# Optimization experiments

Measured on AMD Instinct MI355X. Metric: run time of the kernel, lower is better.

The kernel has to match this reference:

```python
import jax, jax.numpy as jnp
import numpy as np

B, IN_DIM, H, L, P = 256, 64, 768, 4, 8
EPS = 1e-5


def _layernorm(h, g, b):
    mu = jnp.mean(h, axis=-1, keepdims=True)
    var = jnp.mean((h - mu) ** 2, axis=-1, keepdims=True)
    return (h - mu) * jax.lax.rsqrt(var + EPS) * g + b


def setup_inputs() -> dict:
    key = jax.random.key(0)
    ks = jax.random.split(key, 20)
    s_in = 1.0 / np.sqrt(IN_DIM)
    s_h = 1.0 / np.sqrt(H)
    return {
        "x": jax.random.normal(ks[0], (B, IN_DIM), jnp.float32),
        "w_in": jax.random.normal(ks[1], (IN_DIM, H), jnp.float32) * s_in,
        "b_in": jnp.zeros((H,), jnp.float32),
        "ln_g": jnp.ones((L, H), jnp.float32),
        "ln_b": jnp.zeros((L, H), jnp.float32),
        "trop_w": jax.random.normal(ks[2], (L, H, H), jnp.float32) * s_h,  # [L, out, in]
        "trop_b": jnp.zeros((L, H), jnp.float32),
        "lf_amax": jax.random.normal(ks[3], (L, H, P), jnp.float32) * 0.5 + 1.0,
        "lf_bmax": jax.random.normal(ks[4], (L, H, P), jnp.float32) * 0.1,
        "lf_amin": jax.random.normal(ks[5], (L, H, P), jnp.float32) * 0.5 + 1.0,
        "lf_bmin": jax.random.normal(ks[6], (L, H, P), jnp.float32) * 0.1,
        "lf_alpha": jnp.zeros((L, H), jnp.float32),
        "gate_w": jax.random.normal(ks[7], (L, H, H), jnp.float32) * 0.02,
        "gate_b": jnp.full((L, H), 2.0, jnp.float32),
        "cls_w": jax.random.normal(ks[8], (L, H, H), jnp.float32) * s_h,
        "cls_b": jnp.zeros((L, H), jnp.float32),
        "out_g": jnp.ones((H,), jnp.float32),
        "out_b": jnp.zeros((H,), jnp.float32),
        "head_w": jax.random.normal(ks[9], (H, 1), jnp.float32) * s_h,
        "head_b": jnp.zeros((1,), jnp.float32),
    }


def reference(x, w_in, b_in, ln_g, ln_b, trop_w, trop_b, lf_amax, lf_bmax,
              lf_amin, lf_bmin, lf_alpha, gate_w, gate_b, cls_w, cls_b,
              out_g, out_b, head_w, head_b):
    h = x @ w_in + b_in  # [B, H]
    for l in range(L):
        res = h
        hn = _layernorm(h, ln_g[l], ln_b[l])
        # Tropical (max-plus) linear: y[b,o] = max_i(hn[b,i] + W[o,i]) + bias[o]
        t = jnp.max(hn[:, None, :] + trop_w[l][None, :, :], axis=-1) + trop_b[l]
        # LF dual activation: blend of convex (max-plus) and concave (min-plus) PWL
        fmax = jnp.max(t[..., None] * lf_amax[l] + lf_bmax[l], axis=-1)  # [B, H]
        fmin = jnp.min(t[..., None] * lf_amin[l] + lf_bmin[l], axis=-1)
        a = jax.nn.sigmoid(lf_alpha[l])
        trop_out = a * fmax + (1.0 - a) * fmin
        class_out = jax.nn.gelu(hn @ cls_w[l] + cls_b[l], approximate=False)
        g = jax.nn.sigmoid(hn @ gate_w[l] + gate_b[l])
        h = res + g * trop_out + (1.0 - g) * class_out
    h = _layernorm(h, out_g, out_b)
    return (h @ head_w + head_b).squeeze(-1)  # [B]
```

## Files before the change

### kernel.cpp

```cpp
#include <hip/hip_runtime.h>
#include <math.h>

#define HDIM 768
#define BDIM 256
#define INDIM 64
#define NLAYERS 4
#define PDIM 8
#define KSPLIT 16
#define KLEN 48
#define CHK 16
#define TR 128
#define TC 64
#define NTROPBLK 384
#define NCGBLK 96

typedef short bf16x8 __attribute__((ext_vector_type(8)));
typedef float f32x4 __attribute__((ext_vector_type(4)));

__device__ __forceinline__ float sigmoidf_(float x) { return 1.f / (1.f + expf(-x)); }
__device__ __forceinline__ float geluf_(float x) { return 0.5f * x * (1.f + erff(x * 0.70710678118654752f)); }
__device__ __forceinline__ unsigned short f2bf(float f) {
    unsigned int u = __float_as_uint(f);
    u += 0x7FFFu + ((u >> 16) & 1u);
    return (unsigned short)(u >> 16);
}

__device__ __forceinline__ void gload_lds16(const float* g, float* l) {
    __builtin_amdgcn_global_load_lds((const __attribute__((address_space(1))) void*)g,
                                     (__attribute__((address_space(3))) void*)l, 16, 0, 0);
}

__global__ __launch_bounds__(256) void prep_k(const float* __restrict__ trop_w,
                                              const float* __restrict__ cls_w,
                                              const float* __restrict__ gate_w,
                                              float* __restrict__ twT,
                                              unsigned short* __restrict__ wB)
{
    __shared__ float tile[64][65];
    const int z = blockIdx.z;
    const int a0 = blockIdx.x * 64;
    const int b0 = blockIdx.y * 64;
    const int c = threadIdx.x & 63;
    const int r4 = threadIdx.x >> 6;

    if (z < NLAYERS) {
        const float* s = trop_w + (size_t)z * HDIM * HDIM;
        float* d = twT + (size_t)z * HDIM * HDIM;
#pragma unroll
        for (int it = 0; it < 16; ++it) {
            const int r = it * 4 + r4;
            tile[r][c] = s[(size_t)(a0 + r) * HDIM + b0 + c];
        }
        __syncthreads();
#pragma unroll
        for (int it = 0; it < 16; ++it) {
            const int r = it * 4 + r4;
            d[(size_t)(b0 + r) * HDIM + a0 + c] = tile[c][r];
        }
    } else {
        const int zz = z - NLAYERS;
        const int l = zz >> 1, mat = zz & 1;
        const float* s = (mat ? gate_w : cls_w) + (size_t)l * HDIM * HDIM;
        unsigned short* d = wB + (size_t)zz * HDIM * HDIM;
#pragma unroll
        for (int it = 0; it < 16; ++it) {
            const int r = it * 4 + r4;
            tile[r][c] = s[(size_t)(b0 + r) * HDIM + a0 + c];
        }
        __syncthreads();
#pragma unroll
        for (int it = 0; it < 16; ++it) {
            const int r = it * 4 + r4;
            d[(size_t)(a0 + r) * HDIM + b0 + c] = f2bf(tile[c][r]);
        }
    }
}

__global__ __launch_bounds__(256) void input_ln_k(
    const float* __restrict__ x, const float* __restrict__ w_in,
    const float* __restrict__ b_in,
    const float* __restrict__ lng, const float* __restrict__ lnb,
    float* __restrict__ h, float* __restrict__ hnT, unsigned short* __restrict__ hnB)
{
    const int b = blockIdx.x;
    const int t = threadIdx.x;
    __shared__ float xs[INDIM];
    __shared__ float rbuf[8];
    if (t < INDIM) xs[t] = x[b * INDIM + t];
    __syncthreads();

    float acc0 = b_in[t], acc1 = b_in[t + 256], acc2 = b_in[t + 512];
#pragma unroll 8
    for (int i = 0; i < INDIM; ++i) {
        const float xv = xs[i];
        acc0 = fmaf(xv, w_in[i * HDIM + t], acc0);
        acc1 = fmaf(xv, w_in[i * HDIM + t + 256], acc1);
        acc2 = fmaf(xv, w_in[i * HDIM + t + 512], acc2);
    }
    h[(size_t)b * HDIM + t] = acc0;
    h[(size_t)b * HDIM + t + 256] = acc1;
    h[(size_t)b * HDIM + t + 512] = acc2;

    float s = acc0 + acc1 + acc2;
    float q = acc0 * acc0 + acc1 * acc1 + acc2 * acc2;
#pragma unroll
    for (int off = 32; off > 0; off >>= 1) { s += __shfl_down(s, off); q += __shfl_down(q, off); }
    const int wid = t >> 6, lane = t & 63;
    if (lane == 0) { rbuf[wid] = s; rbuf[4 + wid] = q; }
    __syncthreads();
    s = rbuf[0] + rbuf[1] + rbuf[2] + rbuf[3];
    q = rbuf[4] + rbuf[5] + rbuf[6] + rbuf[7];
    const float mu = s * (1.f / HDIM);
    const float var = q * (1.f / HDIM) - mu * mu;
    const float rsig = rsqrtf(var + 1e-5f);

#pragma unroll
    for (int qq = 0; qq < 3; ++qq) {
        const int o = t + qq * 256;
        const float av = (qq == 0) ? acc0 : (qq == 1) ? acc1 : acc2;
        const float v = (av - mu) * rsig * lng[o] + lnb[o];
        hnT[(size_t)o * BDIM + b] = v;
        hnB[(size_t)b * HDIM + o] = f2bf(v);
    }
}

__global__ __launch_bounds__(256, 2) void layer_mm_k(
    const float* __restrict__ hnT,
    const float* __restrict__ twT,
    const unsigned short* __restrict__ hnB,
    const unsigned short* __restrict__ wB,
    float* __restrict__ p_trop, float* __restrict__ p_cls, float* __restrict__ p_gate)
{
    __shared__ float hn_s[2][CHK][TR];
    __shared__ float wt_s[2][CHK][TC];

    const int bx = blockIdx.x;
    const int tid = threadIdx.x;
    const int wave = tid >> 6, lane = tid & 63;

    if (bx < NTROPBLK) {
        const int sp = bx % 24;
        const int slot = bx / 24;
        const int col0 = (sp % 12) * TC;
        const int row0 = (sp / 12) * TR;
        const int k0 = slot * KLEN;

        const int tx = tid & 15, ty = tid >> 4;
        const int r0 = ty * 8, c0 = tx * 4;

        const int hk = lane >> 5;
        const int hcol = (lane & 31) * 4;
        const int wr = lane >> 4;
        const int wcol = (lane & 15) * 4;

        float t_acc[8][4];
#pragma unroll
        for (int i = 0; i < 8; ++i)
#pragma unroll
            for (int j = 0; j < 4; ++j) t_acc[i][j] = -1e30f;

        #define STAGE_T(buf, kb)                                                                   \
        {                                                                                          \
            gload_lds16(hnT + (size_t)((kb) + 4 * wave + hk) * BDIM + row0 + hcol,                 \
                        &hn_s[buf][4 * wave][0]);                                                  \
            gload_lds16(hnT + (size_t)((kb) + 4 * wave + 2 + hk) * BDIM + row0 + hcol,             \
                        &hn_s[buf][4 * wave + 2][0]);                                              \
            gload_lds16(twT + (size_t)((kb) + 4 * wave + wr) * HDIM + col0 + wcol,                 \
                        &wt_s[buf][4 * wave][0]);                                                  \
        }

        STAGE_T(0, k0);
        __builtin_amdgcn_s_waitcnt(0);
        __syncthreads();

        for (int c = 0; c < KLEN / CHK; ++c) {
            const int buf = c & 1;
            if (c + 1 < KLEN / CHK) STAGE_T(1 - buf, k0 + (c + 1) * CHK);
#pragma unroll
            for (int k = 0; k < CHK; ++k) {
                const float4 h0 = *(const float4*)&hn_s[buf][k][r0];
                const float4 h1 = *(const float4*)&hn_s[buf][k][r0 + 4];
                const float4 wt = *(const float4*)&wt_s[buf][k][c0];
                const float hf[8] = {h0.x, h0.y, h0.z, h0.w, h1.x, h1.y, h1.z, h1.w};
                const float wtf[4] = {wt.x, wt.y, wt.z, wt.w};
#pragma unroll
                for (int i = 0; i < 8; ++i)
#pragma unroll
                    for (int j = 0; j < 4; ++j)
                        t_acc[i][j] = fmaxf(t_acc[i][j], hf[i] + wtf[j]);
            }
            __builtin_amdgcn_s_waitcnt(0);
            __syncthreads();
        }
        #undef STAGE_T

        const size_t base = (size_t)slot * BDIM * HDIM;
#pragma unroll
        for (int i = 0; i < 8; ++i) {
            const size_t off = base + (size_t)(row0 + r0 + i) * HDIM + col0 + c0;
            *(float4*)(p_trop + off) = make_float4(t_acc[i][0], t_acc[i][1], t_acc[i][2], t_acc[i][3]);
        }
    } else {
        const int cb = bx - NTROPBLK;
        const int mt = cb & 3, nt = cb >> 2;
        const int m0 = mt * 64 + wave * 16;
        const int n0 = nt * 32;
        const int lm = lane & 15, q = lane >> 4;

        f32x4 acc[2][2];
#pragma unroll
        for (int mat = 0; mat < 2; ++mat)
#pragma unroll
            for (int nn = 0; nn < 2; ++nn) acc[mat][nn] = (f32x4){0.f, 0.f, 0.f, 0.f};

        const unsigned short* aptr = hnB + (size_t)(m0 + lm) * HDIM + q * 8;
        const unsigned short* b00 = wB + (size_t)(n0 + lm) * HDIM + q * 8;
        const unsigned short* b01 = b00 + (size_t)16 * HDIM;
        const unsigned short* b10 = b00 + (size_t)HDIM * HDIM;
        const unsigned short* b11 = b10 + (size_t)16 * HDIM;

#pragma unroll 2
        for (int k0 = 0; k0 < HDIM; k0 += 32) {
            const bf16x8 a  = *(const bf16x8*)(aptr + k0);
            const bf16x8 v00 = *(const bf16x8*)(b00 + k0);
            const bf16x8 v01 = *(const bf16x8*)(b01 + k0);
            const bf16x8 v10 = *(const bf16x8*)(b10 + k0);
            const bf16x8 v11 = *(const bf16x8*)(b11 + k0);
            acc[0][0] = __builtin_amdgcn_mfma_f32_16x16x32_bf16(a, v00, acc[0][0], 0, 0, 0);
            acc[0][1] = __builtin_amdgcn_mfma_f32_16x16x32_bf16(a, v01, acc[0][1], 0, 0, 0);
            acc[1][0] = __builtin_amdgcn_mfma_f32_16x16x32_bf16(a, v10, acc[1][0], 0, 0, 0);
            acc[1][1] = __builtin_amdgcn_mfma_f32_16x16x32_bf16(a, v11, acc[1][1], 0, 0, 0);
        }

#pragma unroll
        for (int nn = 0; nn < 2; ++nn)
#pragma unroll
            for (int r = 0; r < 4; ++r) {
                const size_t off = (size_t)(m0 + q * 4 + r) * HDIM + n0 + nn * 16 + lm;
                p_cls[off]  = acc[0][nn][r];
                p_gate[off] = acc[1][nn][r];
            }
    }
}

__global__ __launch_bounds__(768) void combine_k(
    const float* __restrict__ p_trop, const float* __restrict__ p_cls, const float* __restrict__ p_gate,
    const float* __restrict__ trop_b,
    const float* __restrict__ amax, const float* __restrict__ bmax,
    const float* __restrict__ amin, const float* __restrict__ bmin,
    const float* __restrict__ alpha,
    const float* __restrict__ gate_b, const float* __restrict__ cls_b,
    float* __restrict__ h,
    const float* __restrict__ lng, const float* __restrict__ lnb,
    float* __restrict__ hnT, unsigned short* __restrict__ hnB,
    const float* __restrict__ head_w, const float* __restrict__ head_b,
    float* __restrict__ out, const int is_last)
{
    const int b = blockIdx.x;
    const int o = threadIdx.x;
    __shared__ float rbuf[12], qbuf[12];

    const size_t base = (size_t)b * HDIM + o;
    float tm = -1e30f;
#pragma unroll
    for (int k = 0; k < KSPLIT; ++k)
        tm = fmaxf(tm, p_trop[(size_t)k * BDIM * HDIM + base]);
    const float cs = p_cls[base];
    const float gs = p_gate[base];

    const float tv = tm + trop_b[o];
    float fmx = -1e30f, fmn = 1e30f;
#pragma unroll
    for (int p = 0; p < PDIM; ++p) {
        fmx = fmaxf(fmx, fmaf(tv, amax[o * PDIM + p], bmax[o * PDIM + p]));
        fmn = fminf(fmn, fmaf(tv, amin[o * PDIM + p], bmin[o * PDIM + p]));
    }
    const float a = sigmoidf_(alpha[o]);
    const float trop_out = a * fmx + (1.f - a) * fmn;
    const float cls_out = geluf_(cs + cls_b[o]);
    const float g = sigmoidf_(gs + gate_b[o]);
    const float val = h[base] + g * trop_out + (1.f - g) * cls_out;
    h[base] = val;

    float s = val, q = val * val;
#pragma unroll
    for (int off = 32; off > 0; off >>= 1) { s += __shfl_down(s, off); q += __shfl_down(q, off); }
    const int wid = o >> 6, lane = o & 63;
    if (lane == 0) { rbuf[wid] = s; qbuf[wid] = q; }
    __syncthreads();
    s = 0.f; q = 0.f;
#pragma unroll
    for (int w = 0; w < 12; ++w) { s += rbuf[w]; q += qbuf[w]; }
    const float mu = s * (1.f / HDIM);
    const float var = q * (1.f / HDIM) - mu * mu;
    const float rsig = rsqrtf(var + 1e-5f);
    const float ln_v = (val - mu) * rsig * lng[o] + lnb[o];

    if (!is_last) {
        hnT[(size_t)o * BDIM + b] = ln_v;
        hnB[base] = f2bf(ln_v);
    } else {
        float part = ln_v * head_w[o];
#pragma unroll
        for (int off = 32; off > 0; off >>= 1) part += __shfl_down(part, off);
        __syncthreads();
        if (lane == 0) rbuf[wid] = part;
        __syncthreads();
        if (o == 0) {
            float r = head_b[0];
#pragma unroll
            for (int w = 0; w < 12; ++w) r += rbuf[w];
            out[b] = r;
        }
    }
}

extern "C" void kernel_launch(void* const* d_in, const int* in_sizes, int n_in,
                              void* d_out, int out_size, void* d_ws, size_t ws_size,
                              hipStream_t stream)
{
    const float* x       = (const float*)d_in[0];
    const float* w_in    = (const float*)d_in[1];
    const float* b_in    = (const float*)d_in[2];
    const float* ln_g    = (const float*)d_in[3];
    const float* ln_b    = (const float*)d_in[4];
    const float* trop_w  = (const float*)d_in[5];
    const float* trop_b  = (const float*)d_in[6];
    const float* lf_amax = (const float*)d_in[7];
    const float* lf_bmax = (const float*)d_in[8];
    const float* lf_amin = (const float*)d_in[9];
    const float* lf_bmin = (const float*)d_in[10];
    const float* lf_alpha= (const float*)d_in[11];
    const float* gate_w  = (const float*)d_in[12];
    const float* gate_b  = (const float*)d_in[13];
    const float* cls_w   = (const float*)d_in[14];
    const float* cls_b   = (const float*)d_in[15];
    const float* out_g   = (const float*)d_in[16];
    const float* out_b   = (const float*)d_in[17];
    const float* head_w  = (const float*)d_in[18];
    const float* head_b  = (const float*)d_in[19];
    float* out = (float*)d_out;

    const size_t NBH = (size_t)BDIM * HDIM;
    const size_t WSZ = (size_t)HDIM * HDIM;
    float* ws = (float*)d_ws;
    float* h      = ws;
    float* hnT    = ws + NBH;
    float* twT    = ws + 2 * NBH;
    float* p_trop = twT + (size_t)NLAYERS * WSZ;
    float* p_cls  = p_trop + (size_t)KSPLIT * NBH;
    float* p_gate = p_cls + NBH;
    unsigned short* hnB = (unsigned short*)(p_gate + NBH);
    unsigned short* wB  = hnB + NBH;

    prep_k<<<dim3(12, 12, 12), 256, 0, stream>>>(trop_w, cls_w, gate_w, twT, wB);
    input_ln_k<<<BDIM, 256, 0, stream>>>(x, w_in, b_in, ln_g, ln_b, h, hnT, hnB);

    for (int l = 0; l < NLAYERS; ++l) {
        layer_mm_k<<<NTROPBLK + NCGBLK, 256, 0, stream>>>(
            hnT, twT + (size_t)l * WSZ,
            hnB, wB + (size_t)(2 * l) * WSZ,
            p_trop, p_cls, p_gate);

        const int is_last = (l == NLAYERS - 1);
        combine_k<<<BDIM, 768, 0, stream>>>(
            p_trop, p_cls, p_gate,
            trop_b + (size_t)l * HDIM,
            lf_amax + (size_t)l * HDIM * PDIM, lf_bmax + (size_t)l * HDIM * PDIM,
            lf_amin + (size_t)l * HDIM * PDIM, lf_bmin + (size_t)l * HDIM * PDIM,
            lf_alpha + (size_t)l * HDIM,
            gate_b + (size_t)l * HDIM, cls_b + (size_t)l * HDIM,
            h,
            is_last ? out_g : ln_g + (size_t)(l + 1) * HDIM,
            is_last ? out_b : ln_b + (size_t)(l + 1) * HDIM,
            hnT, hnB, head_w, head_b, out, is_last);
    }
}
```

Measured before the change: 228.1 us.

## Split tropical K range finer and give cls/gate GEMM its own blocks

Raises the tropical max-plus split from 16 to 24 K-chunks of 32, giving 576 tropical blocks, and splits each MFMA block so it computes either the cls or the gate product instead of both, for 192 blocks. The goal is to fill more of the GPU's compute units and shorten the per-block critical path in the layer kernel. In exchange there are more partial tropical slabs for the combine kernel to reduce, and the A operand is loaded twice for the two matrices. This relies on combine_k and the workspace size adapting to the larger KSPLIT.

```diff
diff --git a/kernel.cpp b/kernel.cpp
--- a/kernel.cpp
+++ b/kernel.cpp
@@ -6,13 +6,14 @@
 #define INDIM 64
 #define NLAYERS 4
 #define PDIM 8
-#define KSPLIT 16
-#define KLEN 48
+#define KSPLIT 24
+#define KLEN 32
 #define CHK 16
 #define TR 128
 #define TC 64
-#define NTROPBLK 384
-#define NCGBLK 96
+#define NTROPBLK 576
+#define NCGBLK 192
+#define NBLK (NTROPBLK + NCGBLK)
 
 typedef short bf16x8 __attribute__((ext_vector_type(8)));
 typedef float f32x4 __attribute__((ext_vector_type(4)));
@@ -202,44 +203,38 @@
         }
     } else {
         const int cb = bx - NTROPBLK;
-        const int mt = cb & 3, nt = cb >> 2;
+        const int mat = cb & 1;
+        const int nt = (cb >> 1) % 24;
+        const int mt = cb / 48;
         const int m0 = mt * 64 + wave * 16;
         const int n0 = nt * 32;
         const int lm = lane & 15, q = lane >> 4;
 
-        f32x4 acc[2][2];
-#pragma unroll
-        for (int mat = 0; mat < 2; ++mat)
-#pragma unroll
-            for (int nn = 0; nn < 2; ++nn) acc[mat][nn] = (f32x4){0.f, 0.f, 0.f, 0.f};
+        const unsigned short* wmat = wB + (size_t)mat * HDIM * HDIM;
+        float* pout = mat ? p_gate : p_cls;
+
+        f32x4 acc[2];
+        acc[0] = (f32x4){0.f, 0.f, 0.f, 0.f};
+        acc[1] = (f32x4){0.f, 0.f, 0.f, 0.f};
 
         const unsigned short* aptr = hnB + (size_t)(m0 + lm) * HDIM + q * 8;
-        const unsigned short* b00 = wB + (size_t)(n0 + lm) * HDIM + q * 8;
-        const unsigned short* b01 = b00 + (size_t)16 * HDIM;
-        const unsigned short* b10 = b00 + (size_t)HDIM * HDIM;
-        const unsigned short* b11 = b10 + (size_t)16 * HDIM;
-
-#pragma unroll 2
+        const unsigned short* b0 = wmat + (size_t)(n0 + lm) * HDIM + q * 8;
+        const unsigned short* b1 = b0 + (size_t)16 * HDIM;
+
+#pragma unroll 4
         for (int k0 = 0; k0 < HDIM; k0 += 32) {
             const bf16x8 a  = *(const bf16x8*)(aptr + k0);
-            const bf16x8 v00 = *(const bf16x8*)(b00 + k0);
-            const bf16x8 v01 = *(const bf16x8*)(b01 + k0);
-            const bf16x8 v10 = *(const bf16x8*)(b10 + k0);
-            const bf16x8 v11 = *(const bf16x8*)(b11 + k0);
-            acc[0][0] = __builtin_amdgcn_mfma_f32_16x16x32_bf16(a, v00, acc[0][0], 0, 0, 0);
-            acc[0][1] = __builtin_amdgcn_mfma_f32_16x16x32_bf16(a, v01, acc[0][1], 0, 0, 0);
-            acc[1][0] = __builtin_amdgcn_mfma_f32_16x16x32_bf16(a, v10, acc[1][0], 0, 0, 0);
-            acc[1][1] = __builtin_amdgcn_mfma_f32_16x16x32_bf16(a, v11, acc[1][1], 0, 0, 0);
+            const bf16x8 v0 = *(const bf16x8*)(b0 + k0);
+            const bf16x8 v1 = *(const bf16x8*)(b1 + k0);
+            acc[0] = __builtin_amdgcn_mfma_f32_16x16x32_bf16(a, v0, acc[0], 0, 0, 0);
+            acc[1] = __builtin_amdgcn_mfma_f32_16x16x32_bf16(a, v1, acc[1], 0, 0, 0);
         }
 
 #pragma unroll
         for (int nn = 0; nn < 2; ++nn)
 #pragma unroll
-            for (int r = 0; r < 4; ++r) {
-                const size_t off = (size_t)(m0 + q * 4 + r) * HDIM + n0 + nn * 16 + lm;
-                p_cls[off]  = acc[0][nn][r];
-                p_gate[off] = acc[1][nn][r];
-            }
+            for (int r = 0; r < 4; ++r)
+                pout[(size_t)(m0 + q * 4 + r) * HDIM + n0 + nn * 16 + lm] = acc[nn][r];
     }
 }
 
@@ -357,7 +352,7 @@
     input_ln_k<<<BDIM, 256, 0, stream>>>(x, w_in, b_in, ln_g, ln_b, h, hnT, hnB);
 
     for (int l = 0; l < NLAYERS; ++l) {
-        layer_mm_k<<<NTROPBLK + NCGBLK, 256, 0, stream>>>(
+        layer_mm_k<<<NBLK, 256, 0, stream>>>(
             hnT, twT + (size_t)l * WSZ,
             hnB, wB + (size_t)(2 * l) * WSZ,
             p_trop, p_cls, p_gate);
```

Measured after the change: 217.0 us. 1.05x faster.
